# Kernel tuning notes

Measured on AMD Instinct MI355X. Metric: run time of the kernel, lower is better.

## Reference

```python
import jax, jax.numpy as jnp
import numpy as np

NUM_EMBEDDINGS = 1024
EMBEDDING_DIM = 64
COMMITMENT_COST = 0.25
DECAY = 0.99
EPS = 1e-5


def setup_inputs() -> dict:
    key = jax.random.key(0)
    k1, k2, k3 = jax.random.split(key, 3)
    z = jax.random.normal(k1, (64, EMBEDDING_DIM, 32, 32), dtype=jnp.float32)
    embedding = jax.random.normal(k2, (NUM_EMBEDDINGS, EMBEDDING_DIM), dtype=jnp.float32)
    cluster_size = jnp.zeros((NUM_EMBEDDINGS,), dtype=jnp.float32)
    ema_w = jax.random.normal(k3, (NUM_EMBEDDINGS, EMBEDDING_DIM), dtype=jnp.float32)
    return {"z": z, "embedding": embedding, "cluster_size": cluster_size, "ema_w": ema_w}


def reference(z, embedding, cluster_size, ema_w):
    B, D, H, W = z.shape
    K = embedding.shape[0]
    # (B, H, W, D) -> (N, D)
    z_flat = jnp.transpose(z, (0, 2, 3, 1)).reshape(-1, D)
    # squared L2 distances to every code: (N, K)
    d = (jnp.sum(z_flat * z_flat, axis=1, keepdims=True)
         + jnp.sum(embedding * embedding, axis=1)
         - 2.0 * z_flat @ embedding.T)
    indices = jnp.argmin(d, axis=1)  # (N,)
    z_q = embedding[indices].reshape(B, H, W, D).transpose(0, 3, 1, 2)

    # EMA codebook update (training branch); no gradients flow here in torch (.data ops)
    zf = jax.lax.stop_gradient(z_flat)
    counts = jax.ops.segment_sum(jnp.ones_like(zf[:, 0]), indices, num_segments=K)
    dw = jax.ops.segment_sum(zf, indices, num_segments=K)  # encodings.T @ z_flat
    new_cluster_size = DECAY * cluster_size + (1.0 - DECAY) * counts
    new_ema_w = DECAY * ema_w + (1.0 - DECAY) * dw
    n = jnp.sum(new_cluster_size)
    cs = (new_cluster_size + EPS) / (n + K * EPS) * n
    new_embedding = new_ema_w / cs[:, None]

    loss = COMMITMENT_COST * jnp.mean((z - jax.lax.stop_gradient(z_q)) ** 2)
    z_q_st = z + jax.lax.stop_gradient(z_q - z)  # straight-through
    return (z_q_st, loss, indices.reshape(B, H, W), new_cluster_size, new_ema_w, new_embedding)
```

## Files before the change

### kernel.cpp

```cpp
#include <hip/hip_runtime.h>
#include <stdint.h>

typedef unsigned short ushort;
typedef __attribute__((ext_vector_type(8)))  short bfrag;
typedef __attribute__((ext_vector_type(16))) float f32x16;

#define D      64
#define K      1024
#define HW     1024
#define NROWS  65536
#define NELEM  (NROWS * 64)
#define BAND   0.01f

#define O_ZQ   0
#define O_LOSS 4194304
#define O_IDX  4194305
#define O_NCS  4259841
#define O_EMAW 4260865
#define O_EMB  4326401

#define WB_EH     0x00000
#define WB_EL     0x20000
#define WB_ESQ    0x40000
#define WB_OFFS   0x41000
#define WB_CURSOR 0x42000
#define WB_COUNTS 0x43000
#define WB_LOSSN  0x44000
#define WB_RLIST  0x45000
#define WB_ZF     0x100000
#define WS_NEED_FUSED (0x100000 + 0x1000000)

__device__ __forceinline__ unsigned bf16r(float x) {
    unsigned u = __float_as_uint(x);
    return (u + 0x7FFFu + ((u >> 16) & 1u)) >> 16;
}
__device__ __forceinline__ float bf16f(unsigned h) {
    return __uint_as_float(h << 16);
}

__global__ __launch_bounds__(256) void vq_prep_e(
    const float* __restrict__ emb, ushort* __restrict__ eh,
    ushort* __restrict__ el, float* __restrict__ esq,
    unsigned* __restrict__ zero_region)
{
    const int tid = threadIdx.x;
    if (blockIdx.x == 0) {
#pragma unroll
        for (int i = 0; i < 8; ++i) zero_region[i * 256 + tid] = 0u;
    }
    const int k = blockIdx.x * 4 + (tid >> 6);
    const int d = tid & 63;
    float v = emb[k * 64 + d];
    unsigned hh = bf16r(v);
    float rem = v - bf16f(hh);
    eh[k * 64 + d] = (ushort)hh;
    el[k * 64 + d] = (ushort)bf16r(rem);
    float a = v * v;
#pragma unroll
    for (int off = 32; off; off >>= 1) a += __shfl_xor(a, off);
    if (d == 0) esq[k] = a;
}

__global__ __launch_bounds__(256, 2) void vq_dist_kernel(
    const float* __restrict__ z, const short* __restrict__ eh_g,
    const short* __restrict__ el_g, const float* __restrict__ esq_g,
    float* __restrict__ out, unsigned* __restrict__ counts,
    unsigned* __restrict__ rcnt, int* __restrict__ rlist)
{
    __shared__ __align__(16) short zh_lds[128 * 64];
    __shared__ __align__(16) short zl_lds[128 * 64];
    __shared__ __align__(16) short eh_lds[2][64 * 64];
    __shared__ __align__(16) short el_lds[2][64 * 64];
    __shared__ float esq_lds[1024];

    const int tid  = threadIdx.x;
    const int lane = tid & 63;
    const int wave = tid >> 6;
    const int col  = lane & 31;
    const int h    = lane >> 5;
    const int n0   = blockIdx.x * 128;
    const int b    = n0 >> 10;
    const int hw0  = n0 & 1023;

    for (int it = 0; it < 4; ++it) {
        int task = it * 256 + tid;
        int row  = task & 127;
        int kq   = task >> 7;
        const float* zp = z + (size_t)b * 65536 + (size_t)(kq * 8) * 1024 + hw0 + row;
        bfrag vh, vl;
#pragma unroll
        for (int m = 0; m < 8; ++m) {
            float t = -2.0f * zp[m * 1024];
            unsigned hh = bf16r(t);
            float rem = t - bf16f(hh);
            vh[m] = (short)hh;
            vl[m] = (short)bf16r(rem);
        }
        int unit = kq ^ (row & 7);
        *(bfrag*)&zh_lds[row * 64 + unit * 8] = vh;
        *(bfrag*)&zl_lds[row * 64 + unit * 8] = vl;
    }
    for (int it = 0; it < 4; ++it) {
        int t = it * 256 + tid;
        esq_lds[t] = esq_g[t];
    }

    bfrag pfh[2], pfl[2];
    auto loadE = [&](int cb) {
#pragma unroll
        for (int q = 0; q < 2; ++q) {
            int u = q * 256 + tid;
            int code = u >> 3, m = u & 7;
            pfh[q] = *(const bfrag*)&eh_g[(size_t)(cb + code) * 64 + m * 8];
            pfl[q] = *(const bfrag*)&el_g[(size_t)(cb + code) * 64 + m * 8];
        }
    };
    auto writeE = [&](int buf) {
#pragma unroll
        for (int q = 0; q < 2; ++q) {
            int u = q * 256 + tid;
            int code = u >> 3, m = u & 7;
            int unit = ((code >> 5) * 4 + (m >> 1)) * 64 +
                       ((((m & 1) << 5) | (code & 31)) ^ (m & 7));
            *(bfrag*)&eh_lds[buf][unit * 8] = pfh[q];
            *(bfrag*)&el_lds[buf][unit * 8] = pfl[q];
        }
    };

    loadE(0);
    writeE(0);
    loadE(64);
    __syncthreads();

    const int wrow = wave * 32 + col;
    bfrag zhA[4], zlA[4];
#pragma unroll
    for (int j = 0; j < 4; ++j) {
        int kq = j * 2 + h;
        int unit = kq ^ (wrow & 7);
        zhA[j] = *(const bfrag*)&zh_lds[wrow * 64 + unit * 8];
        zlA[j] = *(const bfrag*)&zl_lds[wrow * 64 + unit * 8];
    }

    float t1s[16], t2s[16];
    unsigned t1c[16];
#pragma unroll
    for (int i = 0; i < 16; ++i) { t1s[i] = INFINITY; t2s[i] = INFINITY; t1c[i] = 0; }

    for (int ch = 0; ch < 16; ++ch) {
        const int cb  = ch * 64;
        const int buf = ch & 1;

        bfrag ehB0[4], elB0[4], ehB1[4], elB1[4];
#pragma unroll
        for (int j = 0; j < 4; ++j) {
            int m = j * 2 + h;
            int sw = (((h << 5) | col) ^ (m & 7));
            ehB0[j] = *(const bfrag*)&eh_lds[buf][(j * 64 + sw) * 8];
            elB0[j] = *(const bfrag*)&el_lds[buf][(j * 64 + sw) * 8];
            ehB1[j] = *(const bfrag*)&eh_lds[buf][((4 + j) * 64 + sw) * 8];
            elB1[j] = *(const bfrag*)&el_lds[buf][((4 + j) * 64 + sw) * 8];
        }
        const float esq0 = esq_lds[cb + col];
        const float esq1 = esq_lds[cb + 32 + col];
        const unsigned c0 = cb + col;
        const unsigned c1 = cb + 32 + col;

        f32x16 acc0, acc1;
#pragma unroll
        for (int i = 0; i < 16; ++i) { acc0[i] = esq0; acc1[i] = esq1; }

        __builtin_amdgcn_s_setprio(1);
#pragma unroll
        for (int j = 0; j < 4; ++j) {
            acc0 = __builtin_amdgcn_mfma_f32_32x32x16_bf16(zhA[j], ehB0[j], acc0, 0, 0, 0);
            acc1 = __builtin_amdgcn_mfma_f32_32x32x16_bf16(zhA[j], ehB1[j], acc1, 0, 0, 0);
        }
#pragma unroll
        for (int j = 0; j < 4; ++j) {
            acc0 = __builtin_amdgcn_mfma_f32_32x32x16_bf16(zhA[j], elB0[j], acc0, 0, 0, 0);
            acc1 = __builtin_amdgcn_mfma_f32_32x32x16_bf16(zhA[j], elB1[j], acc1, 0, 0, 0);
        }
#pragma unroll
        for (int j = 0; j < 4; ++j) {
            acc0 = __builtin_amdgcn_mfma_f32_32x32x16_bf16(zlA[j], ehB0[j], acc0, 0, 0, 0);
            acc1 = __builtin_amdgcn_mfma_f32_32x32x16_bf16(zlA[j], ehB1[j], acc1, 0, 0, 0);
        }
        __builtin_amdgcn_s_setprio(0);

        if (ch < 15) {
            writeE(buf ^ 1);
            if (ch < 14) loadE(cb + 128);
        }

#pragma unroll
        for (int i = 0; i < 16; ++i) {
            float s0 = acc0[i];
            t2s[i] = __builtin_amdgcn_fmed3f(t1s[i], t2s[i], s0);
            bool lt0 = s0 < t1s[i];
            t1s[i] = fminf(t1s[i], s0);
            t1c[i] = lt0 ? c0 : t1c[i];
            float s1 = acc1[i];
            t2s[i] = __builtin_amdgcn_fmed3f(t1s[i], t2s[i], s1);
            bool lt1 = s1 < t1s[i];
            t1s[i] = fminf(t1s[i], s1);
            t1c[i] = lt1 ? c1 : t1c[i];
        }
        __syncthreads();
    }

#pragma unroll
    for (int i = 0; i < 16; ++i) {
        float v = t1s[i], w = t2s[i];
        int   c = (int)t1c[i];
#pragma unroll
        for (int m = 1; m < 32; m <<= 1) {
            float ov = __shfl_xor(v, m);
            int   oc = __shfl_xor(c, m);
            float ow = __shfl_xor(w, m);
            float mx = fmaxf(v, ov);
            w = fminf(fminf(w, ow), mx);
            bool take = (ov < v) || (ov == v && oc < c);
            v = take ? ov : v;
            c = take ? oc : c;
        }
        if ((lane & 31) == 0) {
            int row = (i & 3) + ((i >> 2) << 3) + (h << 2);
            int n = n0 + wave * 32 + row;
            out[O_IDX + n] = (float)c;
            atomicAdd(&counts[c], 1u);
            if (w - v < BAND) {
                unsigned p = atomicAdd(rcnt, 1u);
                rlist[p] = n;
            }
        }
    }
}

__global__ __launch_bounds__(256) void vq_rescore(
    const float* __restrict__ z, const float* __restrict__ emb,
    const float* __restrict__ esq, const unsigned* __restrict__ rcnt,
    const int* __restrict__ rlist, float* __restrict__ out,
    unsigned* __restrict__ counts)
{
    __shared__ float zrow[64];
    __shared__ float rs[4];
    __shared__ int   rc[4];
    const int tid = threadIdx.x;
    const unsigned cnt = rcnt[0];

    for (unsigned i = blockIdx.x; i < cnt; i += gridDim.x) {
        const int n = rlist[i];
        const int b = n >> 10, hw = n & 1023;
        __syncthreads();
        if (tid < 64) zrow[tid] = z[(size_t)b * 65536 + (size_t)tid * 1024 + hw];
        __syncthreads();

        float best = INFINITY; int bc = 0;
        for (int rep = 0; rep < 4; ++rep) {
            int code = rep * 256 + tid;
            const float4* er = (const float4*)(emb + (size_t)code * 64);
            float a0 = 0.f, a1 = 0.f, a2 = 0.f, a3 = 0.f;
#pragma unroll
            for (int q = 0; q < 16; ++q) {
                float4 e = er[q];
                a0 = fmaf(zrow[q * 4 + 0], e.x, a0);
                a1 = fmaf(zrow[q * 4 + 1], e.y, a1);
                a2 = fmaf(zrow[q * 4 + 2], e.z, a2);
                a3 = fmaf(zrow[q * 4 + 3], e.w, a3);
            }
            float s = fmaf(-2.f, (a0 + a1) + (a2 + a3), esq[code]);
            if (s < best || (s == best && code < bc)) { best = s; bc = code; }
        }
        for (int m = 1; m < 64; m <<= 1) {
            float ov = __shfl_xor(best, m);
            int   oc = __shfl_xor(bc, m);
            bool take = (ov < best) || (ov == best && oc < bc);
            best = take ? ov : best;
            bc   = take ? oc : bc;
        }
        if ((tid & 63) == 0) { rs[tid >> 6] = best; rc[tid >> 6] = bc; }
        __syncthreads();
        if (tid == 0) {
            float fb = rs[0]; int fc = rc[0];
#pragma unroll
            for (int q = 1; q < 4; ++q) {
                bool take = (rs[q] < fb) || (rs[q] == fb && rc[q] < fc);
                fb = take ? rs[q] : fb;
                fc = take ? rc[q] : fc;
            }
            int old = (int)out[O_IDX + n];
            if (fc != old) {
                atomicAdd(&counts[old], (unsigned)-1);
                atomicAdd(&counts[fc], 1u);
                out[O_IDX + n] = (float)fc;
            }
        }
    }
}

__global__ __launch_bounds__(1024) void vq_scan_kernel(
    const unsigned* __restrict__ counts, const float* __restrict__ cs,
    unsigned* __restrict__ offs, unsigned* __restrict__ cursor,
    float* __restrict__ out, float* __restrict__ n_val)
{
    __shared__ unsigned wtot[16], wbase[16];
    __shared__ float    fred[16];
    const int k    = threadIdx.x;
    const int lane = k & 63;
    const int w    = k >> 6;

    unsigned c = counts[k];
    unsigned v = c;
#pragma unroll
    for (int off = 1; off < 64; off <<= 1) {
        unsigned t = __shfl_up(v, off);
        if (lane >= off) v += t;
    }
    if (lane == 63) wtot[w] = v;

    float ncs = 0.99f * cs[k] + 0.01f * (float)c;
    out[O_NCS + k] = ncs;
    float s = ncs;
#pragma unroll
    for (int off = 32; off; off >>= 1) s += __shfl_down(s, off);
    if (lane == 0) fred[w] = s;

    __syncthreads();
    if (k == 0) {
        unsigned base = 0; float nt = 0.f;
#pragma unroll
        for (int i = 0; i < 16; ++i) {
            wbase[i] = base;
            base += wtot[i];
            nt += fred[i];
        }
        n_val[0] = nt;
    }
    __syncthreads();
    unsigned o = wbase[w] + (v - c);
    offs[k]   = o;
    cursor[k] = o;
}

__global__ __launch_bounds__(256) void vq_scatter_fused(
    const float* __restrict__ z, const float* __restrict__ emb,
    float* __restrict__ out, float* __restrict__ zf,
    unsigned* __restrict__ cursor, float* __restrict__ loss_acc)
{
    const int tid = threadIdx.x;
    const int n   = blockIdx.x * 256 + tid;
    const int b   = n >> 10;
    const int hw  = n & 1023;
    const int k   = (int)out[O_IDX + n];

    const unsigned pos = atomicAdd(&cursor[k], 1u);
    const float*  zb  = z   + (size_t)b * 65536 + hw;
    float*        oq  = out + O_ZQ + (size_t)b * 65536 + hw;
    const float4* ek4 = (const float4*)emb + (size_t)k * 16;
    float* dst = zf + (size_t)pos * 64;

    float lacc = 0.f;
#pragma unroll
    for (int i = 0; i < 16; ++i) {
        float4 e = ek4[i];
        float z0 = zb[(i * 4 + 0) * 1024];
        float z1 = zb[(i * 4 + 1) * 1024];
        float z2 = zb[(i * 4 + 2) * 1024];
        float z3 = zb[(i * 4 + 3) * 1024];
        *(float4*)&dst[i * 4] = make_float4(z0, z1, z2, z3);
        oq[(i * 4 + 0) * 1024] = z0 + (e.x - z0);
        oq[(i * 4 + 1) * 1024] = z1 + (e.y - z1);
        oq[(i * 4 + 2) * 1024] = z2 + (e.z - z2);
        oq[(i * 4 + 3) * 1024] = z3 + (e.w - z3);
        float d0 = z0 - e.x, d1 = z1 - e.y, d2 = z2 - e.z, d3 = z3 - e.w;
        lacc = fmaf(d0, d0, lacc);
        lacc = fmaf(d1, d1, lacc);
        lacc = fmaf(d2, d2, lacc);
        lacc = fmaf(d3, d3, lacc);
    }

    for (int off = 32; off; off >>= 1) lacc += __shfl_down(lacc, off);
    if ((tid & 63) == 0) atomicAdd(loss_acc, lacc);
}

__global__ __launch_bounds__(256) void vq_scatter_sep(
    const float* __restrict__ z, const float* __restrict__ emb,
    float* __restrict__ out, unsigned* __restrict__ cursor,
    float* __restrict__ loss_acc)
{
    const int tid = threadIdx.x;
    const int n   = blockIdx.x * 256 + tid;
    const int b   = n >> 10;
    const int hw  = n & 1023;
    const int k   = (int)out[O_IDX + n];

    const unsigned pos = atomicAdd(&cursor[k], 1u);
    const float*  zb  = z + (size_t)b * 65536 + hw;
    const float4* ek4 = (const float4*)emb + (size_t)k * 16;
    float* dst = out + O_ZQ + (size_t)pos * 64;

    float lacc = 0.f;
#pragma unroll
    for (int i = 0; i < 16; ++i) {
        float4 e = ek4[i];
        float z0 = zb[(i * 4 + 0) * 1024];
        float z1 = zb[(i * 4 + 1) * 1024];
        float z2 = zb[(i * 4 + 2) * 1024];
        float z3 = zb[(i * 4 + 3) * 1024];
        *(float4*)&dst[i * 4] = make_float4(z0, z1, z2, z3);
        float d0 = z0 - e.x, d1 = z1 - e.y, d2 = z2 - e.z, d3 = z3 - e.w;
        lacc = fmaf(d0, d0, lacc);
        lacc = fmaf(d1, d1, lacc);
        lacc = fmaf(d2, d2, lacc);
        lacc = fmaf(d3, d3, lacc);
    }

    for (int off = 32; off; off >>= 1) lacc += __shfl_down(lacc, off);
    if ((tid & 63) == 0) atomicAdd(loss_acc, lacc);
}

__global__ __launch_bounds__(256) void vq_upd_kernel(
    const float* __restrict__ zf, const unsigned* __restrict__ offs,
    const unsigned* __restrict__ counts, const float* __restrict__ ema_w,
    const float* __restrict__ n_val, const float* __restrict__ loss_acc,
    float* __restrict__ out)
{
    __shared__ float red[4][64];
    const int k   = blockIdx.x;
    const int tid = threadIdx.x;
    const int d   = tid & 63;
    const int q   = tid >> 6;
    const unsigned off = offs[k];
    const unsigned cnt = counts[k];

    float acc = 0.f;
    unsigned j = q;
    for (; j + 12 < cnt; j += 16) {
        float v0 = zf[(size_t)(off + j)      * 64 + d];
        float v1 = zf[(size_t)(off + j + 4)  * 64 + d];
        float v2 = zf[(size_t)(off + j + 8)  * 64 + d];
        float v3 = zf[(size_t)(off + j + 12) * 64 + d];
        acc += v0; acc += v1; acc += v2; acc += v3;
    }
    for (; j < cnt; j += 4) acc += zf[(size_t)(off + j) * 64 + d];

    red[q][d] = acc;
    __syncthreads();
    if (q == 0) {
        float dw = red[0][d] + red[1][d] + red[2][d] + red[3][d];
        float nw = 0.99f * ema_w[k * 64 + d] + 0.01f * dw;
        out[O_EMAW + k * 64 + d] = nw;
        float n   = n_val[0];
        float ncs = out[O_NCS + k];
        float csv = (ncs + 1e-5f) / (n + 1024e-5f) * n;
        out[O_EMB + k * 64 + d] = nw / csv;
    }
    if (k == 0 && tid == 0)
        out[O_LOSS] = 0.25f * loss_acc[0] / (float)NELEM;
}

__global__ __launch_bounds__(256) void vq_zqwrite_kernel(
    const float* __restrict__ z, const float* __restrict__ emb,
    float* __restrict__ out)
{
    const int tid = threadIdx.x;
    const int n   = blockIdx.x * 128 + (tid & 127);
    const int h   = tid >> 7;
    const int b   = n >> 10;
    const int hw  = n & 1023;
    const int k   = (int)out[O_IDX + n];

    const float*  zb  = z   + ((size_t)(b * D + h * 32)) * HW + hw;
    float*        oq  = out + O_ZQ + ((size_t)(b * D + h * 32)) * HW + hw;
    const float4* ek4 = (const float4*)emb + (size_t)k * 16 + h * 8;

#pragma unroll
    for (int i = 0; i < 8; ++i) {
        float4 e = ek4[i];
        float z0 = zb[(i * 4 + 0) * HW];
        float z1 = zb[(i * 4 + 1) * HW];
        float z2 = zb[(i * 4 + 2) * HW];
        float z3 = zb[(i * 4 + 3) * HW];
        oq[(i * 4 + 0) * HW] = z0 + (e.x - z0);
        oq[(i * 4 + 1) * HW] = z1 + (e.y - z1);
        oq[(i * 4 + 2) * HW] = z2 + (e.z - z2);
        oq[(i * 4 + 3) * HW] = z3 + (e.w - z3);
    }
}

extern "C" void kernel_launch(void* const* d_in, const int* in_sizes, int n_in,
                              void* d_out, int out_size, void* d_ws, size_t ws_size,
                              hipStream_t stream) {
    const float* z     = (const float*)d_in[0];
    const float* emb   = (const float*)d_in[1];
    const float* cs    = (const float*)d_in[2];
    const float* ema_w = (const float*)d_in[3];
    float* out = (float*)d_out;

    char* W = (char*)d_ws;
    short*    eh_g   = (short*)(W + WB_EH);
    short*    el_g   = (short*)(W + WB_EL);
    float*    esq    = (float*)(W + WB_ESQ);
    unsigned* offs   = (unsigned*)(W + WB_OFFS);
    unsigned* cursor = (unsigned*)(W + WB_CURSOR);
    unsigned* counts = (unsigned*)(W + WB_COUNTS);
    float*    lossa  = (float*)(W + WB_LOSSN);
    float*    n_val  = lossa + 1;
    unsigned* rcnt   = (unsigned*)(W + WB_LOSSN + 8);
    int*      rlist  = (int*)(W + WB_RLIST);
    float*    zf     = (float*)(W + WB_ZF);

    const bool fused = ws_size >= (size_t)WS_NEED_FUSED;

    vq_prep_e<<<256, 256, 0, stream>>>(emb, (ushort*)eh_g, (ushort*)el_g, esq,
                                       counts);
    vq_dist_kernel<<<512, 256, 0, stream>>>(z, eh_g, el_g, esq, out, counts,
                                            rcnt, rlist);
    vq_rescore<<<128, 256, 0, stream>>>(z, emb, esq, rcnt, rlist, out, counts);
    vq_scan_kernel<<<1, 1024, 0, stream>>>(counts, cs, offs, cursor, out, n_val);
    if (fused) {
        vq_scatter_fused<<<256, 256, 0, stream>>>(z, emb, out, zf, cursor, lossa);
        vq_upd_kernel<<<1024, 256, 0, stream>>>(zf, offs, counts, ema_w,
                                                n_val, lossa, out);
    } else {
        vq_scatter_sep<<<256, 256, 0, stream>>>(z, emb, out, cursor, lossa);
        vq_upd_kernel<<<1024, 256, 0, stream>>>(out + O_ZQ, offs, counts, ema_w,
                                                n_val, lossa, out);
        vq_zqwrite_kernel<<<512, 256, 0, stream>>>(z, emb, out);
    }
}
```

Measured before the change: 215.1 us.

## Split codebook search across two blocks, fold scan into scatter and update kernels

The distance kernel now splits the 1024 codes into two halves handled by separate blocks, doubling the grid, dropping the z staging LDS buffers and raising occupancy to four blocks per CU. A new combine kernel merges the per-half top-2 results and does the argmin, counts and near-tie list. The single-block scan kernel is removed: scatter recomputes prefix offsets in LDS per block, and the update kernel recomputes the offset and total n from counts. Scatter now uses two threads per row. In exchange it adds extra workspace traffic, one extra launch, and redundant per-block scan work.

```diff
diff --git a/kernel.cpp b/kernel.cpp
--- a/kernel.cpp
+++ b/kernel.cpp
@@ -22,13 +22,16 @@
 #define WB_EH     0x00000
 #define WB_EL     0x20000
 #define WB_ESQ    0x40000
-#define WB_OFFS   0x41000
-#define WB_CURSOR 0x42000
 #define WB_COUNTS 0x43000
-#define WB_LOSSN  0x44000
-#define WB_RLIST  0x45000
-#define WB_ZF     0x100000
-#define WS_NEED_FUSED (0x100000 + 0x1000000)
+#define WB_CURSOR 0x44000
+#define WB_LOSSN  0x45000
+#define WB_RLIST  0x46000
+#define WB_T1     0x86000
+#define WB_T2     0x106000
+#define WB_C      0x186000
+#define WS_NEED_SPLIT 0x206000
+#define WB_ZF     0x300000
+#define WS_NEED_FUSED (0x300000 + 0x1000000)
 
 __device__ __forceinline__ unsigned bf16r(float x) {
     unsigned u = __float_as_uint(x);
@@ -46,7 +49,7 @@
     const int tid = threadIdx.x;
     if (blockIdx.x == 0) {
 #pragma unroll
-        for (int i = 0; i < 8; ++i) zero_region[i * 256 + tid] = 0u;
+        for (int i = 0; i < 12; ++i) zero_region[i * 256 + tid] = 0u;
     }
     const int k = blockIdx.x * 4 + (tid >> 6);
     const int d = tid & 63;
@@ -61,49 +64,46 @@
     if (d == 0) esq[k] = a;
 }
 
-__global__ __launch_bounds__(256, 2) void vq_dist_kernel(
+__global__ __launch_bounds__(256, 4) void vq_dist_split(
     const float* __restrict__ z, const short* __restrict__ eh_g,
     const short* __restrict__ el_g, const float* __restrict__ esq_g,
-    float* __restrict__ out, unsigned* __restrict__ counts,
-    unsigned* __restrict__ rcnt, int* __restrict__ rlist)
+    float* __restrict__ ws_t1, float* __restrict__ ws_t2,
+    int* __restrict__ ws_c)
 {
-    __shared__ __align__(16) short zh_lds[128 * 64];
-    __shared__ __align__(16) short zl_lds[128 * 64];
     __shared__ __align__(16) short eh_lds[2][64 * 64];
     __shared__ __align__(16) short el_lds[2][64 * 64];
-    __shared__ float esq_lds[1024];
+    __shared__ float esq_lds[512];
 
     const int tid  = threadIdx.x;
     const int lane = tid & 63;
     const int wave = tid >> 6;
     const int col  = lane & 31;
     const int h    = lane >> 5;
-    const int n0   = blockIdx.x * 128;
-    const int b    = n0 >> 10;
-    const int hw0  = n0 & 1023;
-
-    for (int it = 0; it < 4; ++it) {
-        int task = it * 256 + tid;
-        int row  = task & 127;
-        int kq   = task >> 7;
-        const float* zp = z + (size_t)b * 65536 + (size_t)(kq * 8) * 1024 + hw0 + row;
-        bfrag vh, vl;
+    const int bx     = blockIdx.x;
+    const int split  = bx & 1;
+    const int n0     = (bx >> 1) * 128;
+    const int b      = n0 >> 10;
+    const int hw0    = n0 & 1023;
+    const int cbase0 = split * 512;
+
+    const int wrow = wave * 32 + col;
+    const float* zrow = z + (size_t)b * 65536 + hw0 + wrow;
+    bfrag zhA[4], zlA[4];
+#pragma unroll
+    for (int j = 0; j < 4; ++j) {
+        int kq = j * 2 + h;
 #pragma unroll
         for (int m = 0; m < 8; ++m) {
-            float t = -2.0f * zp[m * 1024];
+            float t = -2.0f * zrow[(size_t)(kq * 8 + m) * 1024];
             unsigned hh = bf16r(t);
-            float rem = t - bf16f(hh);
-            vh[m] = (short)hh;
-            vl[m] = (short)bf16r(rem);
-        }
-        int unit = kq ^ (row & 7);
-        *(bfrag*)&zh_lds[row * 64 + unit * 8] = vh;
-        *(bfrag*)&zl_lds[row * 64 + unit * 8] = vl;
-    }
-    for (int it = 0; it < 4; ++it) {
-        int t = it * 256 + tid;
-        esq_lds[t] = esq_g[t];
-    }
+            zhA[j][m] = (short)hh;
+            zlA[j][m] = (short)bf16r(t - bf16f(hh));
+        }
+    }
+
+#pragma unroll
+    for (int it = 0; it < 2; ++it)
+        esq_lds[it * 256 + tid] = esq_g[cbase0 + it * 256 + tid];
 
     bfrag pfh[2], pfl[2];
     auto loadE = [&](int cb) {
@@ -127,28 +127,18 @@
         }
     };
 
-    loadE(0);
+    loadE(cbase0);
     writeE(0);
-    loadE(64);
+    loadE(cbase0 + 64);
     __syncthreads();
-
-    const int wrow = wave * 32 + col;
-    bfrag zhA[4], zlA[4];
-#pragma unroll
-    for (int j = 0; j < 4; ++j) {
-        int kq = j * 2 + h;
-        int unit = kq ^ (wrow & 7);
-        zhA[j] = *(const bfrag*)&zh_lds[wrow * 64 + unit * 8];
-        zlA[j] = *(const bfrag*)&zl_lds[wrow * 64 + unit * 8];
-    }
 
     float t1s[16], t2s[16];
     unsigned t1c[16];
 #pragma unroll
     for (int i = 0; i < 16; ++i) { t1s[i] = INFINITY; t2s[i] = INFINITY; t1c[i] = 0; }
 
-    for (int ch = 0; ch < 16; ++ch) {
-        const int cb  = ch * 64;
+    for (int ch = 0; ch < 8; ++ch) {
+        const int cb  = cbase0 + ch * 64;
         const int buf = ch & 1;
 
         bfrag ehB0[4], elB0[4], ehB1[4], elB1[4];
@@ -161,8 +151,8 @@
             ehB1[j] = *(const bfrag*)&eh_lds[buf][((4 + j) * 64 + sw) * 8];
             elB1[j] = *(const bfrag*)&el_lds[buf][((4 + j) * 64 + sw) * 8];
         }
-        const float esq0 = esq_lds[cb + col];
-        const float esq1 = esq_lds[cb + 32 + col];
+        const float esq0 = esq_lds[ch * 64 + col];
+        const float esq1 = esq_lds[ch * 64 + 32 + col];
         const unsigned c0 = cb + col;
         const unsigned c1 = cb + 32 + col;
 
@@ -188,9 +178,9 @@
         }
         __builtin_amdgcn_s_setprio(0);
 
-        if (ch < 15) {
+        if (ch < 7) {
             writeE(buf ^ 1);
-            if (ch < 14) loadE(cb + 128);
+            if (ch < 6) loadE(cb + 128);
         }
 
 #pragma unroll
@@ -227,6 +217,201 @@
         if ((lane & 31) == 0) {
             int row = (i & 3) + ((i >> 2) << 3) + (h << 2);
             int n = n0 + wave * 32 + row;
+            ws_t1[split * NROWS + n] = v;
+            ws_t2[split * NROWS + n] = w;
+            ws_c [split * NROWS + n] = c;
+        }
+    }
+}
+
+__global__ __launch_bounds__(256) void vq_combine(
+    const float* __restrict__ ws_t1, const float* __restrict__ ws_t2,
+    const int* __restrict__ ws_c, float* __restrict__ out,
+    unsigned* __restrict__ counts, unsigned* __restrict__ rcnt,
+    int* __restrict__ rlist)
+{
+    const int n = blockIdx.x * 256 + threadIdx.x;
+    float t1a = ws_t1[n],         t1b = ws_t1[NROWS + n];
+    float t2a = ws_t2[n],         t2b = ws_t2[NROWS + n];
+    int   ca  = ws_c[n],          cb  = ws_c[NROWS + n];
+    bool tb = t1b < t1a;
+    float v = tb ? t1b : t1a;
+    int   c = tb ? cb  : ca;
+    float second = fminf(fmaxf(t1a, t1b), tb ? t2b : t2a);
+    out[O_IDX + n] = (float)c;
+    atomicAdd(&counts[c], 1u);
+    if (second - v < BAND) {
+        unsigned p = atomicAdd(rcnt, 1u);
+        rlist[p] = n;
+    }
+}
+
+__global__ __launch_bounds__(256, 2) void vq_dist_mono(
+    const float* __restrict__ z, const short* __restrict__ eh_g,
+    const short* __restrict__ el_g, const float* __restrict__ esq_g,
+    float* __restrict__ out, unsigned* __restrict__ counts,
+    unsigned* __restrict__ rcnt, int* __restrict__ rlist)
+{
+    __shared__ __align__(16) short zh_lds[128 * 64];
+    __shared__ __align__(16) short zl_lds[128 * 64];
+    __shared__ __align__(16) short eh_lds[2][64 * 64];
+    __shared__ __align__(16) short el_lds[2][64 * 64];
+    __shared__ float esq_lds[1024];
+
+    const int tid  = threadIdx.x;
+    const int lane = tid & 63;
+    const int wave = tid >> 6;
+    const int col  = lane & 31;
+    const int h    = lane >> 5;
+    const int n0   = blockIdx.x * 128;
+    const int b    = n0 >> 10;
+    const int hw0  = n0 & 1023;
+
+    for (int it = 0; it < 4; ++it) {
+        int task = it * 256 + tid;
+        int row  = task & 127;
+        int kq   = task >> 7;
+        const float* zp = z + (size_t)b * 65536 + (size_t)(kq * 8) * 1024 + hw0 + row;
+        bfrag vh, vl;
+#pragma unroll
+        for (int m = 0; m < 8; ++m) {
+            float t = -2.0f * zp[m * 1024];
+            unsigned hh = bf16r(t);
+            float rem = t - bf16f(hh);
+            vh[m] = (short)hh;
+            vl[m] = (short)bf16r(rem);
+        }
+        int unit = kq ^ (row & 7);
+        *(bfrag*)&zh_lds[row * 64 + unit * 8] = vh;
+        *(bfrag*)&zl_lds[row * 64 + unit * 8] = vl;
+    }
+    for (int it = 0; it < 4; ++it) {
+        int t = it * 256 + tid;
+        esq_lds[t] = esq_g[t];
+    }
+
+    bfrag pfh[2], pfl[2];
+    auto loadE = [&](int cb) {
+#pragma unroll
+        for (int q = 0; q < 2; ++q) {
+            int u = q * 256 + tid;
+            int code = u >> 3, m = u & 7;
+            pfh[q] = *(const bfrag*)&eh_g[(size_t)(cb + code) * 64 + m * 8];
+            pfl[q] = *(const bfrag*)&el_g[(size_t)(cb + code) * 64 + m * 8];
+        }
+    };
+    auto writeE = [&](int buf) {
+#pragma unroll
+        for (int q = 0; q < 2; ++q) {
+            int u = q * 256 + tid;
+            int code = u >> 3, m = u & 7;
+            int unit = ((code >> 5) * 4 + (m >> 1)) * 64 +
+                       ((((m & 1) << 5) | (code & 31)) ^ (m & 7));
+            *(bfrag*)&eh_lds[buf][unit * 8] = pfh[q];
+            *(bfrag*)&el_lds[buf][unit * 8] = pfl[q];
+        }
+    };
+
+    loadE(0);
+    writeE(0);
+    loadE(64);
+    __syncthreads();
+
+    const int wrow = wave * 32 + col;
+    bfrag zhA[4], zlA[4];
+#pragma unroll
+    for (int j = 0; j < 4; ++j) {
+        int kq = j * 2 + h;
+        int unit = kq ^ (wrow & 7);
+        zhA[j] = *(const bfrag*)&zh_lds[wrow * 64 + unit * 8];
+        zlA[j] = *(const bfrag*)&zl_lds[wrow * 64 + unit * 8];
+    }
+
+    float t1s[16], t2s[16];
+    unsigned t1c[16];
+#pragma unroll
+    for (int i = 0; i < 16; ++i) { t1s[i] = INFINITY; t2s[i] = INFINITY; t1c[i] = 0; }
+
+    for (int ch = 0; ch < 16; ++ch) {
+        const int cb  = ch * 64;
+        const int buf = ch & 1;
+
+        bfrag ehB0[4], elB0[4], ehB1[4], elB1[4];
+#pragma unroll
+        for (int j = 0; j < 4; ++j) {
+            int m = j * 2 + h;
+            int sw = (((h << 5) | col) ^ (m & 7));
+            ehB0[j] = *(const bfrag*)&eh_lds[buf][(j * 64 + sw) * 8];
+            elB0[j] = *(const bfrag*)&el_lds[buf][(j * 64 + sw) * 8];
+            ehB1[j] = *(const bfrag*)&eh_lds[buf][((4 + j) * 64 + sw) * 8];
+            elB1[j] = *(const bfrag*)&el_lds[buf][((4 + j) * 64 + sw) * 8];
+        }
+        const float esq0 = esq_lds[cb + col];
+        const float esq1 = esq_lds[cb + 32 + col];
+        const unsigned c0 = cb + col;
+        const unsigned c1 = cb + 32 + col;
+
+        f32x16 acc0, acc1;
+#pragma unroll
+        for (int i = 0; i < 16; ++i) { acc0[i] = esq0; acc1[i] = esq1; }
+
+        __builtin_amdgcn_s_setprio(1);
+#pragma unroll
+        for (int j = 0; j < 4; ++j) {
+            acc0 = __builtin_amdgcn_mfma_f32_32x32x16_bf16(zhA[j], ehB0[j], acc0, 0, 0, 0);
+            acc1 = __builtin_amdgcn_mfma_f32_32x32x16_bf16(zhA[j], ehB1[j], acc1, 0, 0, 0);
+        }
+#pragma unroll
+        for (int j = 0; j < 4; ++j) {
+            acc0 = __builtin_amdgcn_mfma_f32_32x32x16_bf16(zhA[j], elB0[j], acc0, 0, 0, 0);
+            acc1 = __builtin_amdgcn_mfma_f32_32x32x16_bf16(zhA[j], elB1[j], acc1, 0, 0, 0);
+        }
+#pragma unroll
+        for (int j = 0; j < 4; ++j) {
+            acc0 = __builtin_amdgcn_mfma_f32_32x32x16_bf16(zlA[j], ehB0[j], acc0, 0, 0, 0);
+            acc1 = __builtin_amdgcn_mfma_f32_32x32x16_bf16(zlA[j], ehB1[j], acc1, 0, 0, 0);
+        }
+        __builtin_amdgcn_s_setprio(0);
+
+        if (ch < 15) {
+            writeE(buf ^ 1);
+            if (ch < 14) loadE(cb + 128);
+        }
+
+#pragma unroll
+        for (int i = 0; i < 16; ++i) {
+            float s0 = acc0[i];
+            t2s[i] = __builtin_amdgcn_fmed3f(t1s[i], t2s[i], s0);
+            bool lt0 = s0 < t1s[i];
+            t1s[i] = fminf(t1s[i], s0);
+            t1c[i] = lt0 ? c0 : t1c[i];
+            float s1 = acc1[i];
+            t2s[i] = __builtin_amdgcn_fmed3f(t1s[i], t2s[i], s1);
+            bool lt1 = s1 < t1s[i];
+            t1s[i] = fminf(t1s[i], s1);
+            t1c[i] = lt1 ? c1 : t1c[i];
+        }
+        __syncthreads();
+    }
+
+#pragma unroll
+    for (int i = 0; i < 16; ++i) {
+        float v = t1s[i], w = t2s[i];
+        int   c = (int)t1c[i];
+#pragma unroll
+        for (int m = 1; m < 32; m <<= 1) {
+            float ov = __shfl_xor(v, m);
+            int   oc = __shfl_xor(c, m);
+            float ow = __shfl_xor(w, m);
+            float mx = fmaxf(v, ov);
+            w = fminf(fminf(w, ow), mx);
+            bool take = (ov < v) || (ov == v && oc < c);
+            v = take ? ov : v;
+            c = take ? oc : c;
+        }
+        if ((lane & 31) == 0) {
+            int row = (i & 3) + ((i >> 2) << 3) + (h << 2);
+            int n = n0 + wave * 32 + row;
             out[O_IDX + n] = (float)c;
             atomicAdd(&counts[c], 1u);
             if (w - v < BAND) {
@@ -299,80 +484,72 @@
     }
 }
 
-__global__ __launch_bounds__(1024) void vq_scan_kernel(
-    const unsigned* __restrict__ counts, const float* __restrict__ cs,
-    unsigned* __restrict__ offs, unsigned* __restrict__ cursor,
-    float* __restrict__ out, float* __restrict__ n_val)
+template <bool FUSED>
+__global__ __launch_bounds__(256) void vq_scatter(
+    const float* __restrict__ z, const float* __restrict__ emb,
+    float* __restrict__ out, float* __restrict__ zf,
+    const unsigned* __restrict__ counts, unsigned* __restrict__ cursor,
+    float* __restrict__ lossa)
 {
-    __shared__ unsigned wtot[16], wbase[16];
-    __shared__ float    fred[16];
-    const int k    = threadIdx.x;
-    const int lane = k & 63;
-    const int w    = k >> 6;
-
-    unsigned c = counts[k];
-    unsigned v = c;
+    __shared__ unsigned offs_lds[1024];
+    __shared__ unsigned wt[4], wb[4];
+    const int tid  = threadIdx.x;
+    const int lane = tid & 63;
+    const int wave = tid >> 6;
+
+    unsigned c0 = counts[tid * 4 + 0], c1 = counts[tid * 4 + 1];
+    unsigned c2 = counts[tid * 4 + 2], c3 = counts[tid * 4 + 3];
+    unsigned tot = c0 + c1 + c2 + c3;
+    unsigned v = tot;
 #pragma unroll
     for (int off = 1; off < 64; off <<= 1) {
         unsigned t = __shfl_up(v, off);
         if (lane >= off) v += t;
     }
-    if (lane == 63) wtot[w] = v;
-
-    float ncs = 0.99f * cs[k] + 0.01f * (float)c;
-    out[O_NCS + k] = ncs;
-    float s = ncs;
-#pragma unroll
-    for (int off = 32; off; off >>= 1) s += __shfl_down(s, off);
-    if (lane == 0) fred[w] = s;
-
+    if (lane == 63) wt[wave] = v;
     __syncthreads();
-    if (k == 0) {
-        unsigned base = 0; float nt = 0.f;
-#pragma unroll
-        for (int i = 0; i < 16; ++i) {
-            wbase[i] = base;
-            base += wtot[i];
-            nt += fred[i];
-        }
-        n_val[0] = nt;
+    if (tid == 0) {
+        unsigned base = 0;
+#pragma unroll
+        for (int i = 0; i < 4; ++i) { wb[i] = base; base += wt[i]; }
     }
     __syncthreads();
-    unsigned o = wbase[w] + (v - c);
-    offs[k]   = o;
-    cursor[k] = o;
-}
-
-__global__ __launch_bounds__(256) void vq_scatter_fused(
-    const float* __restrict__ z, const float* __restrict__ emb,
-    float* __restrict__ out, float* __restrict__ zf,
-    unsigned* __restrict__ cursor, float* __restrict__ loss_acc)
-{
-    const int tid = threadIdx.x;
-    const int n   = blockIdx.x * 256 + tid;
-    const int b   = n >> 10;
-    const int hw  = n & 1023;
-    const int k   = (int)out[O_IDX + n];
-
-    const unsigned pos = atomicAdd(&cursor[k], 1u);
-    const float*  zb  = z   + (size_t)b * 65536 + hw;
-    float*        oq  = out + O_ZQ + (size_t)b * 65536 + hw;
-    const float4* ek4 = (const float4*)emb + (size_t)k * 16;
-    float* dst = zf + (size_t)pos * 64;
+    unsigned ex = wb[wave] + (v - tot);
+    offs_lds[tid * 4 + 0] = ex;
+    offs_lds[tid * 4 + 1] = ex + c0;
+    offs_lds[tid * 4 + 2] = ex + c0 + c1;
+    offs_lds[tid * 4 + 3] = ex + c0 + c1 + c2;
+    __syncthreads();
+
+    const int gt = blockIdx.x * 256 + tid;
+    const int n  = gt >> 1;
+    const int h  = gt & 1;
+    const int b  = n >> 10, hw = n & 1023;
+    const int k  = (int)out[O_IDX + n];
+    unsigned pos = 0;
+    if (h == 0) pos = offs_lds[k] + atomicAdd(&cursor[k], 1u);
+    pos = __shfl(pos, lane & 62);
+
+    const float*  zb  = z + (size_t)b * 65536 + (size_t)h * 32768 + hw;
+    const float4* ek4 = (const float4*)emb + (size_t)k * 16 + h * 8;
+    float* dst = (FUSED ? zf : out + O_ZQ) + (size_t)pos * 64 + h * 32;
+    float* oq  = out + O_ZQ + (size_t)b * 65536 + (size_t)h * 32768 + hw;
 
     float lacc = 0.f;
 #pragma unroll
-    for (int i = 0; i < 16; ++i) {
+    for (int i = 0; i < 8; ++i) {
         float4 e = ek4[i];
         float z0 = zb[(i * 4 + 0) * 1024];
         float z1 = zb[(i * 4 + 1) * 1024];
         float z2 = zb[(i * 4 + 2) * 1024];
         float z3 = zb[(i * 4 + 3) * 1024];
         *(float4*)&dst[i * 4] = make_float4(z0, z1, z2, z3);
-        oq[(i * 4 + 0) * 1024] = z0 + (e.x - z0);
-        oq[(i * 4 + 1) * 1024] = z1 + (e.y - z1);
-        oq[(i * 4 + 2) * 1024] = z2 + (e.z - z2);
-        oq[(i * 4 + 3) * 1024] = z3 + (e.w - z3);
+        if (FUSED) {
+            oq[(i * 4 + 0) * 1024] = z0 + (e.x - z0);
+            oq[(i * 4 + 1) * 1024] = z1 + (e.y - z1);
+            oq[(i * 4 + 2) * 1024] = z2 + (e.z - z2);
+            oq[(i * 4 + 3) * 1024] = z3 + (e.w - z3);
+        }
         float d0 = z0 - e.x, d1 = z1 - e.y, d2 = z2 - e.z, d3 = z3 - e.w;
         lacc = fmaf(d0, d0, lacc);
         lacc = fmaf(d1, d1, lacc);
@@ -381,69 +558,53 @@
     }
 
     for (int off = 32; off; off >>= 1) lacc += __shfl_down(lacc, off);
-    if ((tid & 63) == 0) atomicAdd(loss_acc, lacc);
-}
-
-__global__ __launch_bounds__(256) void vq_scatter_sep(
-    const float* __restrict__ z, const float* __restrict__ emb,
-    float* __restrict__ out, unsigned* __restrict__ cursor,
-    float* __restrict__ loss_acc)
+    if ((tid & 63) == 0) atomicAdd(lossa, lacc);
+}
+
+__global__ __launch_bounds__(256) void vq_upd_kernel(
+    const float* __restrict__ zsrc, const unsigned* __restrict__ counts,
+    const float* __restrict__ cs, const float* __restrict__ ema_w,
+    const float* __restrict__ lossa, float* __restrict__ out)
 {
-    const int tid = threadIdx.x;
-    const int n   = blockIdx.x * 256 + tid;
-    const int b   = n >> 10;
-    const int hw  = n & 1023;
-    const int k   = (int)out[O_IDX + n];
-
-    const unsigned pos = atomicAdd(&cursor[k], 1u);
-    const float*  zb  = z + (size_t)b * 65536 + hw;
-    const float4* ek4 = (const float4*)emb + (size_t)k * 16;
-    float* dst = out + O_ZQ + (size_t)pos * 64;
-
-    float lacc = 0.f;
-#pragma unroll
-    for (int i = 0; i < 16; ++i) {
-        float4 e = ek4[i];
-        float z0 = zb[(i * 4 + 0) * 1024];
-        float z1 = zb[(i * 4 + 1) * 1024];
-        float z2 = zb[(i * 4 + 2) * 1024];
-        float z3 = zb[(i * 4 + 3) * 1024];
-        *(float4*)&dst[i * 4] = make_float4(z0, z1, z2, z3);
-        float d0 = z0 - e.x, d1 = z1 - e.y, d2 = z2 - e.z, d3 = z3 - e.w;
-        lacc = fmaf(d0, d0, lacc);
-        lacc = fmaf(d1, d1, lacc);
-        lacc = fmaf(d2, d2, lacc);
-        lacc = fmaf(d3, d3, lacc);
-    }
-
-    for (int off = 32; off; off >>= 1) lacc += __shfl_down(lacc, off);
-    if ((tid & 63) == 0) atomicAdd(loss_acc, lacc);
-}
-
-__global__ __launch_bounds__(256) void vq_upd_kernel(
-    const float* __restrict__ zf, const unsigned* __restrict__ offs,
-    const unsigned* __restrict__ counts, const float* __restrict__ ema_w,
-    const float* __restrict__ n_val, const float* __restrict__ loss_acc,
-    float* __restrict__ out)
-{
-    __shared__ float red[4][64];
-    const int k   = blockIdx.x;
-    const int tid = threadIdx.x;
-    const int d   = tid & 63;
-    const int q   = tid >> 6;
-    const unsigned off = offs[k];
+    __shared__ float    red[4][64];
+    __shared__ float    nr[4];
+    __shared__ unsigned orr[4];
+    const int k    = blockIdx.x;
+    const int tid  = threadIdx.x;
+    const int lane = tid & 63;
+    const int wave = tid >> 6;
+    const int d    = tid & 63;
+    const int q    = tid >> 6;
+
+    float    npart = 0.f;
+    unsigned opart = 0;
+#pragma unroll
+    for (int it = 0; it < 4; ++it) {
+        int j = it * 256 + tid;
+        unsigned cj = counts[j];
+        npart += 0.99f * cs[j] + 0.01f * (float)cj;
+        if (j < k) opart += cj;
+    }
+#pragma unroll
+    for (int off = 32; off; off >>= 1) {
+        npart += __shfl_down(npart, off);
+        opart += __shfl_down(opart, off);
+    }
+    if (lane == 0) { nr[wave] = npart; orr[wave] = opart; }
+    __syncthreads();
+    const float    n   = (nr[0] + nr[1]) + (nr[2] + nr[3]);
+    const unsigned off = orr[0] + orr[1] + orr[2] + orr[3];
     const unsigned cnt = counts[k];
 
     float acc = 0.f;
     unsigned j = q;
     for (; j + 12 < cnt; j += 16) {
-        float v0 = zf[(size_t)(off + j)      * 64 + d];
-        float v1 = zf[(size_t)(off + j + 4)  * 64 + d];
-        float v2 = zf[(size_t)(off + j + 8)  * 64 + d];
-        float v3 = zf[(size_t)(off + j + 12) * 64 + d];
-        acc += v0; acc += v1; acc += v2; acc += v3;
-    }
-    for (; j < cnt; j += 4) acc += zf[(size_t)(off + j) * 64 + d];
+        acc += zsrc[(size_t)(off + j)      * 64 + d];
+        acc += zsrc[(size_t)(off + j + 4)  * 64 + d];
+        acc += zsrc[(size_t)(off + j + 8)  * 64 + d];
+        acc += zsrc[(size_t)(off + j + 12) * 64 + d];
+    }
+    for (; j < cnt; j += 4) acc += zsrc[(size_t)(off + j) * 64 + d];
 
     red[q][d] = acc;
     __syncthreads();
@@ -451,13 +612,13 @@
         float dw = red[0][d] + red[1][d] + red[2][d] + red[3][d];
         float nw = 0.99f * ema_w[k * 64 + d] + 0.01f * dw;
         out[O_EMAW + k * 64 + d] = nw;
-        float n   = n_val[0];
-        float ncs = out[O_NCS + k];
+        float ncs = 0.99f * cs[k] + 0.01f * (float)cnt;
         float csv = (ncs + 1e-5f) / (n + 1024e-5f) * n;
         out[O_EMB + k * 64 + d] = nw / csv;
+        if (d == 0) out[O_NCS + k] = ncs;
     }
     if (k == 0 && tid == 0)
-        out[O_LOSS] = 0.25f * loss_acc[0] / (float)NELEM;
+        out[O_LOSS] = 0.25f * lossa[0] / (float)NELEM;
 }
 
 __global__ __launch_bounds__(256) void vq_zqwrite_kernel(
@@ -471,21 +632,21 @@
     const int hw  = n & 1023;
     const int k   = (int)out[O_IDX + n];
 
-    const float*  zb  = z   + ((size_t)(b * D + h * 32)) * HW + hw;
-    float*        oq  = out + O_ZQ + ((size_t)(b * D + h * 32)) * HW + hw;
+    const float*  zb  = z   + (size_t)b * 65536 + (size_t)h * 32768 + hw;
+    float*        oq  = out + O_ZQ + (size_t)b * 65536 + (size_t)h * 32768 + hw;
     const float4* ek4 = (const float4*)emb + (size_t)k * 16 + h * 8;
 
 #pragma unroll
     for (int i = 0; i < 8; ++i) {
         float4 e = ek4[i];
-        float z0 = zb[(i * 4 + 0) * HW];
-        float z1 = zb[(i * 4 + 1) * HW];
-        float z2 = zb[(i * 4 + 2) * HW];
-        float z3 = zb[(i * 4 + 3) * HW];
-        oq[(i * 4 + 0) * HW] = z0 + (e.x - z0);
-        oq[(i * 4 + 1) * HW] = z1 + (e.y - z1);
-        oq[(i * 4 + 2) * HW] = z2 + (e.z - z2);
-        oq[(i * 4 + 3) * HW] = z3 + (e.w - z3);
+        float z0 = zb[(i * 4 + 0) * 1024];
+        float z1 = zb[(i * 4 + 1) * 1024];
+        float z2 = zb[(i * 4 + 2) * 1024];
+        float z3 = zb[(i * 4 + 3) * 1024];
+        oq[(i * 4 + 0) * 1024] = z0 + (e.x - z0);
+        oq[(i * 4 + 1) * 1024] = z1 + (e.y - z1);
+        oq[(i * 4 + 2) * 1024] = z2 + (e.z - z2);
+        oq[(i * 4 + 3) * 1024] = z3 + (e.w - z3);
     }
 }
 
@@ -502,31 +663,41 @@
     short*    eh_g   = (short*)(W + WB_EH);
     short*    el_g   = (short*)(W + WB_EL);
     float*    esq    = (float*)(W + WB_ESQ);
-    unsigned* offs   = (unsigned*)(W + WB_OFFS);
+    unsigned* counts = (unsigned*)(W + WB_COUNTS);
     unsigned* cursor = (unsigned*)(W + WB_CURSOR);
-    unsigned* counts = (unsigned*)(W + WB_COUNTS);
     float*    lossa  = (float*)(W + WB_LOSSN);
-    float*    n_val  = lossa + 1;
-    unsigned* rcnt   = (unsigned*)(W + WB_LOSSN + 8);
+    unsigned* rcnt   = (unsigned*)(W + WB_LOSSN + 0x100);
     int*      rlist  = (int*)(W + WB_RLIST);
+    float*    ws_t1  = (float*)(W + WB_T1);
+    float*    ws_t2  = (float*)(W + WB_T2);
+    int*      ws_c   = (int*)(W + WB_C);
     float*    zf     = (float*)(W + WB_ZF);
 
+    const bool split = ws_size >= (size_t)WS_NEED_SPLIT;
     const bool fused = ws_size >= (size_t)WS_NEED_FUSED;
 
     vq_prep_e<<<256, 256, 0, stream>>>(emb, (ushort*)eh_g, (ushort*)el_g, esq,
                                        counts);
-    vq_dist_kernel<<<512, 256, 0, stream>>>(z, eh_g, el_g, esq, out, counts,
+    if (split) {
+        vq_dist_split<<<1024, 256, 0, stream>>>(z, eh_g, el_g, esq,
+                                                ws_t1, ws_t2, ws_c);
+        vq_combine<<<256, 256, 0, stream>>>(ws_t1, ws_t2, ws_c, out, counts,
                                             rcnt, rlist);
-    vq_rescore<<<128, 256, 0, stream>>>(z, emb, esq, rcnt, rlist, out, counts);
-    vq_scan_kernel<<<1, 1024, 0, stream>>>(counts, cs, offs, cursor, out, n_val);
+    } else {
+        vq_dist_mono<<<512, 256, 0, stream>>>(z, eh_g, el_g, esq, out, counts,
+                                              rcnt, rlist);
+    }
+    vq_rescore<<<256, 256, 0, stream>>>(z, emb, esq, rcnt, rlist, out, counts);
     if (fused) {
-        vq_scatter_fused<<<256, 256, 0, stream>>>(z, emb, out, zf, cursor, lossa);
-        vq_upd_kernel<<<1024, 256, 0, stream>>>(zf, offs, counts, ema_w,
-                                                n_val, lossa, out);
+        vq_scatter<true><<<512, 256, 0, stream>>>(z, emb, out, zf, counts,
+                                                  cursor, lossa);
+        vq_upd_kernel<<<1024, 256, 0, stream>>>(zf, counts, cs, ema_w, lossa,
+                                                out);
     } else {
-        vq_scatter_sep<<<256, 256, 0, stream>>>(z, emb, out, cursor, lossa);
-        vq_upd_kernel<<<1024, 256, 0, stream>>>(out + O_ZQ, offs, counts, ema_w,
-                                                n_val, lossa, out);
+        vq_scatter<false><<<512, 256, 0, stream>>>(z, emb, out, zf, counts,
+                                                   cursor, lossa);
+        vq_upd_kernel<<<1024, 256, 0, stream>>>(out + O_ZQ, counts, cs, ema_w,
+                                                lossa, out);
         vq_zqwrite_kernel<<<512, 256, 0, stream>>>(z, emb, out);
     }
 }
```

New measurement: 529.4 us. 2.46x slower.
